# Performance work log

Hardware: AMD Instinct MI355X
Metric: run time of the kernel (lower is better)

Reference implementation:

```python
import jax, jax.numpy as jnp
import numpy as np

N = 20000
E = 640000
IN_DIM = 128
HID = 128
OUT = 64


def setup_inputs() -> dict:
    key = jax.random.key(0)
    ks = jax.random.split(key, 16)
    s = 0.05
    inp = {
        'feat': jax.random.normal(ks[0], (N, IN_DIM), jnp.float32),
        'edge_index': jax.random.randint(ks[1], (2, E), 0, N, jnp.int64),
        # GCNConv params
        'W_gcn': jax.random.normal(ks[2], (IN_DIM, HID), jnp.float32) * s,
        'b_gcn': jnp.zeros((HID,), jnp.float32),
        # SAGEConv params (lin_l: aggregated neighbors w/ bias; lin_r: root, no bias)
        'W_sage_l': jax.random.normal(ks[3], (HID, HID), jnp.float32) * s,
        'b_sage_l': jnp.zeros((HID,), jnp.float32),
        'W_sage_r': jax.random.normal(ks[4], (HID, HID), jnp.float32) * s,
        # policy MLP
        'W1': jax.random.normal(ks[5], (HID, HID), jnp.float32) * s,
        'b1': jnp.zeros((HID,), jnp.float32),
        'W2': jax.random.normal(ks[6], (HID, HID), jnp.float32) * s,
        'b2': jnp.zeros((HID,), jnp.float32),
        'W3': jax.random.normal(ks[7], (HID, OUT), jnp.float32) * s,
        'b3': jnp.zeros((OUT,), jnp.float32),
        # value head
        'Wv': jax.random.normal(ks[8], (HID, 1), jnp.float32) * s,
        'bv': jnp.zeros((1,), jnp.float32),
    }
    return inp


def _gcn(feat, src, dst, W, b):
    # PyG GCNConv: add self loops, sym-normalize by deg^-1/2 on both ends
    loop = jnp.arange(N, dtype=src.dtype)
    s = jnp.concatenate([src, loop])
    d = jnp.concatenate([dst, loop])
    deg = jax.ops.segment_sum(jnp.ones_like(d, jnp.float32), d, num_segments=N)
    dinv = jnp.where(deg > 0, jax.lax.rsqrt(deg), 0.0)
    x = feat @ W  # [N, HID]
    msg = x[s] * (dinv[s] * dinv[d])[:, None]  # [E+N, HID]
    return jax.ops.segment_sum(msg, d, num_segments=N) + b


def _sage_mean(h, src, dst, Wl, bl, Wr):
    # PyG SAGEConv(aggr='mean'): lin_l(mean_neigh) + lin_r(root)
    neigh_sum = jax.ops.segment_sum(h[src], dst, num_segments=N)
    cnt = jax.ops.segment_sum(jnp.ones_like(dst, jnp.float32), dst, num_segments=N)
    mean = neigh_sum / jnp.maximum(cnt, 1.0)[:, None]
    return mean @ Wl + bl + h @ Wr


def reference(feat, edge_index, W_gcn, b_gcn, W_sage_l, b_sage_l, W_sage_r,
              W1, b1, W2, b2, W3, b3, Wv, bv):
    src, dst = edge_index[0], edge_index[1]
    h = jax.nn.relu(_gcn(feat, src, dst, W_gcn, b_gcn))
    h = jax.nn.relu(_sage_mean(h, src, dst, W_sage_l, b_sage_l, W_sage_r))
    # policy MLP (GELU exact, matching torch nn.GELU default)
    z = jax.nn.gelu(h @ W1 + b1, approximate=False)
    z = jax.nn.gelu(z @ W2 + b2, approximate=False)
    means = z @ W3 + b3  # [N, OUT]
    values = (h @ Wv + bv)[:, 0]  # [N]
    return (means, values)
```

## Files before the change

kernel.cpp:

```cpp
#include <hip/hip_runtime.h>
#include <math.h>


typedef __attribute__((ext_vector_type(8))) short short8;
typedef __attribute__((ext_vector_type(4))) float floatx4;

__device__ __forceinline__ unsigned short f2b(float f) {
    unsigned u = __float_as_uint(f);
    unsigned r = (u + 0x7fffu + ((u >> 16) & 1u)) >> 16;
    return (unsigned short)r;
}
__device__ __forceinline__ float b2f(unsigned short h) {
    return __uint_as_float(((unsigned)h) << 16);
}
__device__ __forceinline__ float b2f_lo(unsigned v) {
    return __uint_as_float(v << 16);
}
__device__ __forceinline__ float b2f_hi(unsigned v) {
    return __uint_as_float(v & 0xffff0000u);
}
__device__ __forceinline__ floatx4 MFMA(short8 a, short8 b, floatx4 c) {
    return __builtin_amdgcn_mfma_f32_16x16x32_bf16(a, b, c, 0, 0, 0);
}
__device__ __forceinline__ float gelu_exact(float x) {
    return 0.5f * x * (1.0f + erff(x * 0.70710678118654752440f));
}

#define FRAG(P, ct, ks, lane) (*(const short8*)((P) + (((((ct)*4 + (ks))*64) + (lane)) << 3)))


__global__ __launch_bounds__(256) void count_pack_kernel(
    const int* __restrict__ eidx, int E,
    int* __restrict__ cnt, int* __restrict__ rank,
    const float* Wg, const float* Wsl, const float* Wsr,
    const float* W1, const float* W2, const float* W3,
    unsigned short* Pg, unsigned short* Psl, unsigned short* Psr,
    unsigned short* P1, unsigned short* P2, unsigned short* P3,
    int countBlocks)
{
    if ((int)blockIdx.x < countBlocks) {
        int e = blockIdx.x * 256 + threadIdx.x;
        if (e < E) {
            int d = eidx[E + e];
            rank[e] = atomicAdd(&cnt[d], 1);
        }
        return;
    }
    int t = (blockIdx.x - countBlocks) * 256 + threadIdx.x;
    const float* W; unsigned short* P; int NC = 128; int base;
    if (t < 2048)       { W = Wg;  P = Pg;  base = t; }
    else if (t < 4096)  { W = Wsl; P = Psl; base = t - 2048; }
    else if (t < 6144)  { W = Wsr; P = Psr; base = t - 4096; }
    else if (t < 8192)  { W = W1;  P = P1;  base = t - 6144; }
    else if (t < 10240) { W = W2;  P = P2;  base = t - 8192; }
    else if (t < 11264) { W = W3;  P = P3;  base = t - 10240; NC = 64; }
    else return;
    int l  = base & 63;
    int ks = (base >> 6) & 3;
    int ct = base >> 8;
    int n  = ct * 16 + (l & 15);
    int k0 = ks * 32 + ((l >> 4) << 3);
    short8 v;
    #pragma unroll
    for (int j = 0; j < 8; j++) v[j] = (short)f2b(W[(size_t)(k0 + j) * NC + n]);
    *(short8*)(P + ((size_t)base << 3)) = v;
}


__global__ __launch_bounds__(256) void scan_kernel(
    const int* __restrict__ cnt, int N,
    int* __restrict__ row_ptr, int* __restrict__ bsums,
    float* __restrict__ dinv)
{
    __shared__ int sh[256];
    int b = blockIdx.x, tid = threadIdx.x;
    int i0 = b * 1024 + tid * 4;
    int v0 = (i0 + 0 < N) ? cnt[i0 + 0] : 0;
    int v1 = (i0 + 1 < N) ? cnt[i0 + 1] : 0;
    int v2 = (i0 + 2 < N) ? cnt[i0 + 2] : 0;
    int v3 = (i0 + 3 < N) ? cnt[i0 + 3] : 0;
    int tot = v0 + v1 + v2 + v3;
    sh[tid] = tot;
    __syncthreads();
    for (int off = 1; off < 256; off <<= 1) {
        int t = (tid >= off) ? sh[tid - off] : 0;
        __syncthreads();
        sh[tid] += t;
        __syncthreads();
    }
    int excl = sh[tid] - tot;
    if (i0 + 0 < N) { row_ptr[i0 + 0] = excl;                dinv[i0 + 0] = rsqrtf((float)(v0 + 1)); }
    if (i0 + 1 < N) { row_ptr[i0 + 1] = excl + v0;           dinv[i0 + 1] = rsqrtf((float)(v1 + 1)); }
    if (i0 + 2 < N) { row_ptr[i0 + 2] = excl + v0 + v1;      dinv[i0 + 2] = rsqrtf((float)(v2 + 1)); }
    if (i0 + 3 < N) { row_ptr[i0 + 3] = excl + v0 + v1 + v2; dinv[i0 + 3] = rsqrtf((float)(v3 + 1)); }
    if (tid == 255) bsums[b] = sh[255];
}


__global__ __launch_bounds__(256) void fill_gemm_kernel(
    const int* __restrict__ eidx, const int* __restrict__ rank,
    const int* __restrict__ row_ptr, const int* __restrict__ bsums,
    int E, int* __restrict__ col,
    const float* __restrict__ feat, const unsigned short* __restrict__ Pg,
    unsigned short* __restrict__ xs, int M, int fillBlocks)
{
    if ((int)blockIdx.x < fillBlocks) {
        int e = blockIdx.x * 256 + threadIdx.x;
        if (e < E) {
            int d = eidx[E + e];
            int b = d >> 10;
            int off = 0;
            for (int j = 0; j < b; j++) off += bsums[j];
            col[off + row_ptr[d] + rank[e]] = eidx[e];
        }
        return;
    }
    int bid = blockIdx.x - fillBlocks;
    int w = bid * 4 + (threadIdx.x >> 6);
    if (w >= (M / 16) * 2) return;
    int lane = threadIdx.x & 63;
    int m = lane & 15, quad = lane >> 4;
    int rt = w >> 1, ch = w & 1;
    const float* arow = feat + (size_t)(rt * 16 + m) * 128;
    short8 a[4];
    #pragma unroll
    for (int ks = 0; ks < 4; ks++) {
        float4 f0 = *(const float4*)(arow + ks * 32 + quad * 8);
        float4 f1 = *(const float4*)(arow + ks * 32 + quad * 8 + 4);
        short8 s;
        s[0] = (short)f2b(f0.x); s[1] = (short)f2b(f0.y);
        s[2] = (short)f2b(f0.z); s[3] = (short)f2b(f0.w);
        s[4] = (short)f2b(f1.x); s[5] = (short)f2b(f1.y);
        s[6] = (short)f2b(f1.z); s[7] = (short)f2b(f1.w);
        a[ks] = s;
    }
    #pragma unroll
    for (int ct = 0; ct < 4; ct++) {
        floatx4 acc = {0.f, 0.f, 0.f, 0.f};
        #pragma unroll
        for (int ks = 0; ks < 4; ks++)
            acc = MFMA(a[ks], FRAG(Pg, ch * 4 + ct, ks, lane), acc);
        #pragma unroll
        for (int reg = 0; reg < 4; reg++)
            xs[(size_t)(rt * 16 + quad * 4 + reg) * 128 + (ch * 4 + ct) * 16 + m] =
                f2b(acc[reg]);
    }
}


template<bool GCN>
__global__ __launch_bounds__(256) void agg_kernel(
    const unsigned short* __restrict__ X, const int* __restrict__ row_ptr,
    const int* __restrict__ bsums, const int* __restrict__ col,
    const float* __restrict__ dinv, const float* __restrict__ bias,
    unsigned short* __restrict__ Y, int N, int E)
{
    int w = (int)((blockIdx.x * 256 + threadIdx.x) >> 6);
    if (w >= N) return;
    int lane = threadIdx.x & 63;
    int g = lane >> 4, t = lane & 15;
    const uint4* Xq = (const uint4*)X;

    int b = w >> 10;
    int off = 0;
    for (int j = 0; j < b; j++) off += bsums[j];
    int beg = off + row_ptr[w];
    int end;
    if (w + 1 < N) {
        int off2 = (((w + 1) >> 10) != b) ? off + bsums[b] : off;
        end = off2 + row_ptr[w + 1];
    } else end = E;
    int deg = end - beg;

    float acc[8] = {0.f, 0.f, 0.f, 0.f, 0.f, 0.f, 0.f, 0.f};

    for (int base = beg; base < end; base += 64) {
        int rem = end - base;
        int n = rem < 64 ? rem : 64;
        int idx = (lane < n) ? col[base + lane] : 0;
        for (int j0 = 0; j0 < n; j0 += 16) {
            #pragma unroll
            for (int u = 0; u < 4; u++) {
                int j = j0 + u * 4 + g;
                int s = __shfl(idx, j & 63);
                if (j < n) {
                    uint4 q = Xq[(size_t)s * 16 + t];
                    float sc = GCN ? dinv[s] : 1.0f;
                    acc[0] = fmaf(b2f_lo(q.x), sc, acc[0]);
                    acc[1] = fmaf(b2f_hi(q.x), sc, acc[1]);
                    acc[2] = fmaf(b2f_lo(q.y), sc, acc[2]);
                    acc[3] = fmaf(b2f_hi(q.y), sc, acc[3]);
                    acc[4] = fmaf(b2f_lo(q.z), sc, acc[4]);
                    acc[5] = fmaf(b2f_hi(q.z), sc, acc[5]);
                    acc[6] = fmaf(b2f_lo(q.w), sc, acc[6]);
                    acc[7] = fmaf(b2f_hi(q.w), sc, acc[7]);
                }
            }
        }
    }
    #pragma unroll
    for (int i = 0; i < 8; i++) {
        acc[i] += __shfl_xor(acc[i], 16);
        acc[i] += __shfl_xor(acc[i], 32);
    }
    if (g == 0) {
        float out[8];
        if (GCN) {
            float dw = dinv[w];
            uint4 q = Xq[(size_t)w * 16 + t];
            acc[0] = fmaf(b2f_lo(q.x), dw, acc[0]);
            acc[1] = fmaf(b2f_hi(q.x), dw, acc[1]);
            acc[2] = fmaf(b2f_lo(q.y), dw, acc[2]);
            acc[3] = fmaf(b2f_hi(q.y), dw, acc[3]);
            acc[4] = fmaf(b2f_lo(q.z), dw, acc[4]);
            acc[5] = fmaf(b2f_hi(q.z), dw, acc[5]);
            acc[6] = fmaf(b2f_lo(q.w), dw, acc[6]);
            acc[7] = fmaf(b2f_hi(q.w), dw, acc[7]);
            float4 b0 = *(const float4*)(bias + t * 8);
            float4 b1 = *(const float4*)(bias + t * 8 + 4);
            out[0] = fmaxf(fmaf(acc[0], dw, b0.x), 0.f);
            out[1] = fmaxf(fmaf(acc[1], dw, b0.y), 0.f);
            out[2] = fmaxf(fmaf(acc[2], dw, b0.z), 0.f);
            out[3] = fmaxf(fmaf(acc[3], dw, b0.w), 0.f);
            out[4] = fmaxf(fmaf(acc[4], dw, b1.x), 0.f);
            out[5] = fmaxf(fmaf(acc[5], dw, b1.y), 0.f);
            out[6] = fmaxf(fmaf(acc[6], dw, b1.z), 0.f);
            out[7] = fmaxf(fmaf(acc[7], dw, b1.w), 0.f);
        } else {
            float rc = 1.0f / (float)(deg > 0 ? deg : 1);
            #pragma unroll
            for (int i = 0; i < 8; i++) out[i] = acc[i] * rc;
        }
        uint4 r;
        r.x = (unsigned)f2b(out[0]) | ((unsigned)f2b(out[1]) << 16);
        r.y = (unsigned)f2b(out[2]) | ((unsigned)f2b(out[3]) << 16);
        r.z = (unsigned)f2b(out[4]) | ((unsigned)f2b(out[5]) << 16);
        r.w = (unsigned)f2b(out[6]) | ((unsigned)f2b(out[7]) << 16);
        ((uint4*)Y)[(size_t)w * 16 + t] = r;
    }
}


__global__ __launch_bounds__(256) void sage_mlp_kernel(
    const unsigned short* __restrict__ mean, const unsigned short* __restrict__ h1,
    const unsigned short* __restrict__ Psl, const unsigned short* __restrict__ Psr,
    const float* __restrict__ bsl,
    const unsigned short* __restrict__ P1, const float* __restrict__ b1,
    const unsigned short* __restrict__ P2, const float* __restrict__ b2,
    const unsigned short* __restrict__ P3, const float* __restrict__ b3,
    const float* __restrict__ Wv, const float* __restrict__ bv,
    float* __restrict__ means, float* __restrict__ values, int M)
{
    __shared__ unsigned short z[4][16 * 136];
    int widx = threadIdx.x >> 6, lane = threadIdx.x & 63;
    int w = blockIdx.x * 4 + widx;
    if (w >= M / 16) return;
    int m = lane & 15, quad = lane >> 4;
    unsigned short* zt = &z[widx][0];
    int r0 = w * 16;

    short8 am[4], ar[4];
    #pragma unroll
    for (int ks = 0; ks < 4; ks++) {
        am[ks] = *(const short8*)(mean + (size_t)(r0 + m) * 128 + ks * 32 + quad * 8);
        ar[ks] = *(const short8*)(h1   + (size_t)(r0 + m) * 128 + ks * 32 + quad * 8);
    }

    float vpart[4] = {0.f, 0.f, 0.f, 0.f};
    #pragma unroll
    for (int ct = 0; ct < 8; ct++) {
        floatx4 acc = {0.f, 0.f, 0.f, 0.f};
        #pragma unroll
        for (int ks = 0; ks < 4; ks++) acc = MFMA(am[ks], FRAG(Psl, ct, ks, lane), acc);
        #pragma unroll
        for (int ks = 0; ks < 4; ks++) acc = MFMA(ar[ks], FRAG(Psr, ct, ks, lane), acc);
        float bb = bsl[ct * 16 + m];
        float wv = Wv[ct * 16 + m];
        #pragma unroll
        for (int reg = 0; reg < 4; reg++) {
            float o = fmaxf(acc[reg] + bb, 0.f);
            vpart[reg] = fmaf(o, wv, vpart[reg]);
            zt[(quad * 4 + reg) * 136 + ct * 16 + m] = f2b(o);
        }
    }
    #pragma unroll
    for (int off = 1; off <= 8; off <<= 1) {
        #pragma unroll
        for (int reg = 0; reg < 4; reg++)
            vpart[reg] += __shfl_xor(vpart[reg], off);
    }
    if (m == 0) {
        float bvv = bv[0];
        #pragma unroll
        for (int reg = 0; reg < 4; reg++)
            values[r0 + quad * 4 + reg] = vpart[reg] + bvv;
    }

    short8 a1[4];
    #pragma unroll
    for (int ks = 0; ks < 4; ks++)
        a1[ks] = *(const short8*)(zt + m * 136 + ks * 32 + quad * 8);

    #pragma unroll
    for (int ct = 0; ct < 8; ct++) {
        floatx4 acc = {0.f, 0.f, 0.f, 0.f};
        #pragma unroll
        for (int ks = 0; ks < 4; ks++) acc = MFMA(a1[ks], FRAG(P1, ct, ks, lane), acc);
        float bb = b1[ct * 16 + m];
        #pragma unroll
        for (int reg = 0; reg < 4; reg++)
            zt[(quad * 4 + reg) * 136 + ct * 16 + m] = f2b(gelu_exact(acc[reg] + bb));
    }
    short8 a2[4];
    #pragma unroll
    for (int ks = 0; ks < 4; ks++)
        a2[ks] = *(const short8*)(zt + m * 136 + ks * 32 + quad * 8);

    #pragma unroll
    for (int ct = 0; ct < 8; ct++) {
        floatx4 acc = {0.f, 0.f, 0.f, 0.f};
        #pragma unroll
        for (int ks = 0; ks < 4; ks++) acc = MFMA(a2[ks], FRAG(P2, ct, ks, lane), acc);
        float bb = b2[ct * 16 + m];
        #pragma unroll
        for (int reg = 0; reg < 4; reg++)
            zt[(quad * 4 + reg) * 136 + ct * 16 + m] = f2b(gelu_exact(acc[reg] + bb));
    }
    short8 a3[4];
    #pragma unroll
    for (int ks = 0; ks < 4; ks++)
        a3[ks] = *(const short8*)(zt + m * 136 + ks * 32 + quad * 8);

    #pragma unroll
    for (int ct = 0; ct < 4; ct++) {
        floatx4 acc = {0.f, 0.f, 0.f, 0.f};
        #pragma unroll
        for (int ks = 0; ks < 4; ks++) acc = MFMA(a3[ks], FRAG(P3, ct, ks, lane), acc);
        float bb = b3[ct * 16 + m];
        #pragma unroll
        for (int reg = 0; reg < 4; reg++)
            means[(size_t)(r0 + quad * 4 + reg) * 64 + ct * 16 + m] = acc[reg] + bb;
    }
}


extern "C" void kernel_launch(void* const* d_in, const int* in_sizes, int n_in,
                              void* d_out, int out_size, void* d_ws, size_t ws_size,
                              hipStream_t stream) {
    const float* feat  = (const float*)d_in[0];
    const int*   eidx  = (const int*)d_in[1];
    const float* W_gcn = (const float*)d_in[2];
    const float* b_gcn = (const float*)d_in[3];
    const float* W_sl  = (const float*)d_in[4];
    const float* b_sl  = (const float*)d_in[5];
    const float* W_sr  = (const float*)d_in[6];
    const float* W1    = (const float*)d_in[7];
    const float* b1    = (const float*)d_in[8];
    const float* W2    = (const float*)d_in[9];
    const float* b2    = (const float*)d_in[10];
    const float* W3    = (const float*)d_in[11];
    const float* b3    = (const float*)d_in[12];
    const float* Wv    = (const float*)d_in[13];
    const float* bv    = (const float*)d_in[14];

    const int N = in_sizes[0] / 128;
    const int E = in_sizes[1] / 2;

    char* ws = (char*)d_ws;
    size_t off = 0;
    auto alloc = [&](size_t bytes) -> void* {
        void* p = ws + off;
        off += (bytes + 255) & ~(size_t)255;
        return p;
    };
    int*   cnt     = (int*)alloc((size_t)N * 4);
    int*   rank    = (int*)alloc((size_t)E * 4);
    int*   row_ptr = (int*)alloc((size_t)N * 4);
    int*   bsums   = (int*)alloc(32 * 4);
    float* dinv    = (float*)alloc((size_t)N * 4);
    int*   col     = (int*)alloc((size_t)E * 4);
    unsigned short* xs   = (unsigned short*)alloc((size_t)N * 128 * 2);
    unsigned short* h1   = (unsigned short*)alloc((size_t)N * 128 * 2);
    unsigned short* mean = (unsigned short*)alloc((size_t)N * 128 * 2);
    unsigned short* Pg   = (unsigned short*)alloc(2048 * 8 * 2);
    unsigned short* Psl  = (unsigned short*)alloc(2048 * 8 * 2);
    unsigned short* Psr  = (unsigned short*)alloc(2048 * 8 * 2);
    unsigned short* P1   = (unsigned short*)alloc(2048 * 8 * 2);
    unsigned short* P2   = (unsigned short*)alloc(2048 * 8 * 2);
    unsigned short* P3   = (unsigned short*)alloc(1024 * 8 * 2);

    hipMemsetAsync(cnt, 0, (size_t)N * 4, stream);

    const int countBlocks = (E + 255) / 256;
    const int packBlocks  = (11264 + 255) / 256;
    count_pack_kernel<<<countBlocks + packBlocks, 256, 0, stream>>>(
        eidx, E, cnt, rank, W_gcn, W_sl, W_sr, W1, W2, W3,
        Pg, Psl, Psr, P1, P2, P3, countBlocks);

    const int NB = (N + 1023) / 1024;
    scan_kernel<<<NB, 256, 0, stream>>>(cnt, N, row_ptr, bsums, dinv);

    const int fillBlocks = (E + 255) / 256;
    const int gemmBlocks = ((N / 16) * 2 + 3) / 4;
    fill_gemm_kernel<<<fillBlocks + gemmBlocks, 256, 0, stream>>>(
        eidx, rank, row_ptr, bsums, E, col, feat, Pg, xs, N, fillBlocks);

    const int agrid = (N + 3) / 4;
    agg_kernel<true><<<agrid, 256, 0, stream>>>(xs, row_ptr, bsums, col, dinv, b_gcn, h1, N, E);
    agg_kernel<false><<<agrid, 256, 0, stream>>>(h1, row_ptr, bsums, col, dinv, nullptr, mean, N, E);

    sage_mlp_kernel<<<(N / 16 + 3) / 4, 256, 0, stream>>>(
        mean, h1, Psl, Psr, b_sl, P1, b1, P2, b2, P3, b3, Wv, bv,
        (float*)d_out, (float*)d_out + (size_t)N * 64, N);
}
```

Before: 201.6 us.

## Fuse scan into count kernel, prescale GCN source features, simplify aggregation loop

Merges the degree scan into the count/pack kernel using a last-block-done atomic, and builds the CSR with atomic cursors instead of per-edge ranks plus block offsets. The source-side dinv scaling is folded into the feature GEMM output, so the aggregation loop becomes plain adds with no per-edge dinv gather. The aggregation loop is also rewritten to issue two independent row loads per iteration without shuffles, and row_ptr gets an N+1 sentinel so the per-row offset summation goes away. The costs are a single-block serial scan at the tail of the first kernel, non-deterministic column order within each row, and bf16 rounding applied after the dinv scaling.

Result: slower. 415.9 us (+106.3%).

```diff
diff --git a/kernel.cpp b/kernel.cpp
--- a/kernel.cpp
+++ b/kernel.cpp
@@ -29,89 +29,96 @@
 #define FRAG(P, ct, ks, lane) (*(const short8*)((P) + (((((ct)*4 + (ks))*64) + (lane)) << 3)))
 
 
-__global__ __launch_bounds__(256) void count_pack_kernel(
-    const int* __restrict__ eidx, int E,
-    int* __restrict__ cnt, int* __restrict__ rank,
+__global__ __launch_bounds__(256) void count_pack_scan_kernel(
+    const int* __restrict__ eidx, int E, int N,
+    int* __restrict__ cnt, int* __restrict__ done,
+    int* __restrict__ row_ptr, int* __restrict__ cursor, float* __restrict__ dinv,
     const float* Wg, const float* Wsl, const float* Wsr,
     const float* W1, const float* W2, const float* W3,
     unsigned short* Pg, unsigned short* Psl, unsigned short* Psr,
     unsigned short* P1, unsigned short* P2, unsigned short* P3,
-    int countBlocks)
+    int countBlocks, int totalBlocks)
 {
+    __shared__ int sh[256];
+    __shared__ int isLast;
+
     if ((int)blockIdx.x < countBlocks) {
         int e = blockIdx.x * 256 + threadIdx.x;
-        if (e < E) {
-            int d = eidx[E + e];
-            rank[e] = atomicAdd(&cnt[d], 1);
+        if (e < E) atomicAdd(&cnt[eidx[E + e]], 1);
+    } else {
+        int t = (blockIdx.x - countBlocks) * 256 + threadIdx.x;
+        if (t < 11264) {
+            const float* W; unsigned short* P; int NC = 128; int base;
+            if (t < 2048)       { W = Wg;  P = Pg;  base = t; }
+            else if (t < 4096)  { W = Wsl; P = Psl; base = t - 2048; }
+            else if (t < 6144)  { W = Wsr; P = Psr; base = t - 4096; }
+            else if (t < 8192)  { W = W1;  P = P1;  base = t - 6144; }
+            else if (t < 10240) { W = W2;  P = P2;  base = t - 8192; }
+            else                { W = W3;  P = P3;  base = t - 10240; NC = 64; }
+            int l  = base & 63;
+            int ks = (base >> 6) & 3;
+            int ct = base >> 8;
+            int n  = ct * 16 + (l & 15);
+            int k0 = ks * 32 + ((l >> 4) << 3);
+            short8 v;
+            #pragma unroll
+            for (int j = 0; j < 8; j++) v[j] = (short)f2b(W[(size_t)(k0 + j) * NC + n]);
+            *(short8*)(P + ((size_t)base << 3)) = v;
         }
-        return;
-    }
-    int t = (blockIdx.x - countBlocks) * 256 + threadIdx.x;
-    const float* W; unsigned short* P; int NC = 128; int base;
-    if (t < 2048)       { W = Wg;  P = Pg;  base = t; }
-    else if (t < 4096)  { W = Wsl; P = Psl; base = t - 2048; }
-    else if (t < 6144)  { W = Wsr; P = Psr; base = t - 4096; }
-    else if (t < 8192)  { W = W1;  P = P1;  base = t - 6144; }
-    else if (t < 10240) { W = W2;  P = P2;  base = t - 8192; }
-    else if (t < 11264) { W = W3;  P = P3;  base = t - 10240; NC = 64; }
-    else return;
-    int l  = base & 63;
-    int ks = (base >> 6) & 3;
-    int ct = base >> 8;
-    int n  = ct * 16 + (l & 15);
-    int k0 = ks * 32 + ((l >> 4) << 3);
-    short8 v;
-    #pragma unroll
-    for (int j = 0; j < 8; j++) v[j] = (short)f2b(W[(size_t)(k0 + j) * NC + n]);
-    *(short8*)(P + ((size_t)base << 3)) = v;
-}
-
-
-__global__ __launch_bounds__(256) void scan_kernel(
-    const int* __restrict__ cnt, int N,
-    int* __restrict__ row_ptr, int* __restrict__ bsums,
-    float* __restrict__ dinv)
-{
-    __shared__ int sh[256];
-    int b = blockIdx.x, tid = threadIdx.x;
-    int i0 = b * 1024 + tid * 4;
-    int v0 = (i0 + 0 < N) ? cnt[i0 + 0] : 0;
-    int v1 = (i0 + 1 < N) ? cnt[i0 + 1] : 0;
-    int v2 = (i0 + 2 < N) ? cnt[i0 + 2] : 0;
-    int v3 = (i0 + 3 < N) ? cnt[i0 + 3] : 0;
-    int tot = v0 + v1 + v2 + v3;
-    sh[tid] = tot;
+    }
+
+    __threadfence();
+    __syncthreads();
+    if (threadIdx.x == 0)
+        isLast = (atomicAdd(done, 1) == totalBlocks - 1) ? 1 : 0;
+    __syncthreads();
+    if (!isLast) return;
+    __threadfence();
+
+    int tid = threadIdx.x;
+    int CH = (N + 255) >> 8;
+    int t0 = tid * CH;
+    int sum = 0;
+    for (int i = 0; i < CH; i++) {
+        int idx = t0 + i;
+        if (idx < N) sum += cnt[idx];
+    }
+    sh[tid] = sum;
     __syncthreads();
     for (int off = 1; off < 256; off <<= 1) {
-        int t = (tid >= off) ? sh[tid - off] : 0;
+        int v = (tid >= off) ? sh[tid - off] : 0;
         __syncthreads();
-        sh[tid] += t;
+        sh[tid] += v;
         __syncthreads();
     }
-    int excl = sh[tid] - tot;
-    if (i0 + 0 < N) { row_ptr[i0 + 0] = excl;                dinv[i0 + 0] = rsqrtf((float)(v0 + 1)); }
-    if (i0 + 1 < N) { row_ptr[i0 + 1] = excl + v0;           dinv[i0 + 1] = rsqrtf((float)(v1 + 1)); }
-    if (i0 + 2 < N) { row_ptr[i0 + 2] = excl + v0 + v1;      dinv[i0 + 2] = rsqrtf((float)(v2 + 1)); }
-    if (i0 + 3 < N) { row_ptr[i0 + 3] = excl + v0 + v1 + v2; dinv[i0 + 3] = rsqrtf((float)(v3 + 1)); }
-    if (tid == 255) bsums[b] = sh[255];
+    int run = sh[tid] - sum;
+    for (int i = 0; i < CH; i++) {
+        int idx = t0 + i;
+        if (idx < N) {
+            int c = cnt[idx];
+            row_ptr[idx] = run;
+            cursor[idx]  = run;
+            dinv[idx] = rsqrtf((float)(c + 1));
+            run += c;
+        }
+    }
+    if (tid == 0) row_ptr[N] = E;
 }
 
 
 __global__ __launch_bounds__(256) void fill_gemm_kernel(
-    const int* __restrict__ eidx, const int* __restrict__ rank,
-    const int* __restrict__ row_ptr, const int* __restrict__ bsums,
-    int E, int* __restrict__ col,
-    const float* __restrict__ feat, const unsigned short* __restrict__ Pg,
+    const int* __restrict__ eidx, int E,
+    int* __restrict__ cursor, int* __restrict__ col,
+    const float* __restrict__ feat, const float* __restrict__ dinv,
+    const unsigned short* __restrict__ Pg,
     unsigned short* __restrict__ xs, int M, int fillBlocks)
 {
     if ((int)blockIdx.x < fillBlocks) {
         int e = blockIdx.x * 256 + threadIdx.x;
         if (e < E) {
             int d = eidx[E + e];
-            int b = d >> 10;
-            int off = 0;
-            for (int j = 0; j < b; j++) off += bsums[j];
-            col[off + row_ptr[d] + rank[e]] = eidx[e];
+            int pos = atomicAdd(&cursor[d], 1);
+            col[pos] = eidx[e];
         }
         return;
     }
@@ -134,6 +141,8 @@
         s[6] = (short)f2b(f1.z); s[7] = (short)f2b(f1.w);
         a[ks] = s;
     }
+    float4 dvv = *(const float4*)(dinv + rt * 16 + quad * 4);
+    float dv[4] = {dvv.x, dvv.y, dvv.z, dvv.w};
     #pragma unroll
     for (int ct = 0; ct < 4; ct++) {
         floatx4 acc = {0.f, 0.f, 0.f, 0.f};
@@ -143,7 +152,7 @@
         #pragma unroll
         for (int reg = 0; reg < 4; reg++)
             xs[(size_t)(rt * 16 + quad * 4 + reg) * 128 + (ch * 4 + ct) * 16 + m] =
-                f2b(acc[reg]);
+                f2b(acc[reg] * dv[reg]);
     }
 }
 
@@ -151,9 +160,9 @@
 template<bool GCN>
 __global__ __launch_bounds__(256) void agg_kernel(
     const unsigned short* __restrict__ X, const int* __restrict__ row_ptr,
-    const int* __restrict__ bsums, const int* __restrict__ col,
-    const float* __restrict__ dinv, const float* __restrict__ bias,
-    unsigned short* __restrict__ Y, int N, int E)
+    const int* __restrict__ col, const float* __restrict__ dinv,
+    const float* __restrict__ bias,
+    unsigned short* __restrict__ Y, int N)
 {
     int w = (int)((blockIdx.x * 256 + threadIdx.x) >> 6);
     if (w >= N) return;
@@ -161,43 +170,35 @@
     int g = lane >> 4, t = lane & 15;
     const uint4* Xq = (const uint4*)X;
 
-    int b = w >> 10;
-    int off = 0;
-    for (int j = 0; j < b; j++) off += bsums[j];
-    int beg = off + row_ptr[w];
-    int end;
-    if (w + 1 < N) {
-        int off2 = (((w + 1) >> 10) != b) ? off + bsums[b] : off;
-        end = off2 + row_ptr[w + 1];
-    } else end = E;
+    int beg = row_ptr[w], end = row_ptr[w + 1];
     int deg = end - beg;
 
     float acc[8] = {0.f, 0.f, 0.f, 0.f, 0.f, 0.f, 0.f, 0.f};
 
-    for (int base = beg; base < end; base += 64) {
-        int rem = end - base;
-        int n = rem < 64 ? rem : 64;
-        int idx = (lane < n) ? col[base + lane] : 0;
-        for (int j0 = 0; j0 < n; j0 += 16) {
-            #pragma unroll
-            for (int u = 0; u < 4; u++) {
-                int j = j0 + u * 4 + g;
-                int s = __shfl(idx, j & 63);
-                if (j < n) {
-                    uint4 q = Xq[(size_t)s * 16 + t];
-                    float sc = GCN ? dinv[s] : 1.0f;
-                    acc[0] = fmaf(b2f_lo(q.x), sc, acc[0]);
-                    acc[1] = fmaf(b2f_hi(q.x), sc, acc[1]);
-                    acc[2] = fmaf(b2f_lo(q.y), sc, acc[2]);
-                    acc[3] = fmaf(b2f_hi(q.y), sc, acc[3]);
-                    acc[4] = fmaf(b2f_lo(q.z), sc, acc[4]);
-                    acc[5] = fmaf(b2f_hi(q.z), sc, acc[5]);
-                    acc[6] = fmaf(b2f_lo(q.w), sc, acc[6]);
-                    acc[7] = fmaf(b2f_hi(q.w), sc, acc[7]);
-                }
-            }
-        }
-    }
+    int e = beg + g;
+    for (; e + 4 < end; e += 8) {
+        int s0 = col[e];
+        int s1 = col[e + 4];
+        uint4 q0 = Xq[(size_t)s0 * 16 + t];
+        uint4 q1 = Xq[(size_t)s1 * 16 + t];
+        acc[0] += b2f_lo(q0.x); acc[1] += b2f_hi(q0.x);
+        acc[2] += b2f_lo(q0.y); acc[3] += b2f_hi(q0.y);
+        acc[4] += b2f_lo(q0.z); acc[5] += b2f_hi(q0.z);
+        acc[6] += b2f_lo(q0.w); acc[7] += b2f_hi(q0.w);
+        acc[0] += b2f_lo(q1.x); acc[1] += b2f_hi(q1.x);
+        acc[2] += b2f_lo(q1.y); acc[3] += b2f_hi(q1.y);
+        acc[4] += b2f_lo(q1.z); acc[5] += b2f_hi(q1.z);
+        acc[6] += b2f_lo(q1.w); acc[7] += b2f_hi(q1.w);
+    }
+    if (e < end) {
+        int s0 = col[e];
+        uint4 q0 = Xq[(size_t)s0 * 16 + t];
+        acc[0] += b2f_lo(q0.x); acc[1] += b2f_hi(q0.x);
+        acc[2] += b2f_lo(q0.y); acc[3] += b2f_hi(q0.y);
+        acc[4] += b2f_lo(q0.z); acc[5] += b2f_hi(q0.z);
+        acc[6] += b2f_lo(q0.w); acc[7] += b2f_hi(q0.w);
+    }
+
     #pragma unroll
     for (int i = 0; i < 8; i++) {
         acc[i] += __shfl_xor(acc[i], 16);
@@ -208,14 +209,10 @@
         if (GCN) {
             float dw = dinv[w];
             uint4 q = Xq[(size_t)w * 16 + t];
-            acc[0] = fmaf(b2f_lo(q.x), dw, acc[0]);
-            acc[1] = fmaf(b2f_hi(q.x), dw, acc[1]);
-            acc[2] = fmaf(b2f_lo(q.y), dw, acc[2]);
-            acc[3] = fmaf(b2f_hi(q.y), dw, acc[3]);
-            acc[4] = fmaf(b2f_lo(q.z), dw, acc[4]);
-            acc[5] = fmaf(b2f_hi(q.z), dw, acc[5]);
-            acc[6] = fmaf(b2f_lo(q.w), dw, acc[6]);
-            acc[7] = fmaf(b2f_hi(q.w), dw, acc[7]);
+            acc[0] += b2f_lo(q.x); acc[1] += b2f_hi(q.x);
+            acc[2] += b2f_lo(q.y); acc[3] += b2f_hi(q.y);
+            acc[4] += b2f_lo(q.z); acc[5] += b2f_hi(q.z);
+            acc[6] += b2f_lo(q.w); acc[7] += b2f_hi(q.w);
             float4 b0 = *(const float4*)(bias + t * 8);
             float4 b1 = *(const float4*)(bias + t * 8 + 4);
             out[0] = fmaxf(fmaf(acc[0], dw, b0.x), 0.f);
@@ -373,10 +370,10 @@
         off += (bytes + 255) & ~(size_t)255;
         return p;
     };
-    int*   cnt     = (int*)alloc((size_t)N * 4);
-    int*   rank    = (int*)alloc((size_t)E * 4);
-    int*   row_ptr = (int*)alloc((size_t)N * 4);
-    int*   bsums   = (int*)alloc(32 * 4);
+    int*   cnt     = (int*)alloc((size_t)(N + 64) * 4);
+    int*   done    = cnt + N;
+    int*   row_ptr = (int*)alloc((size_t)(N + 1) * 4);
+    int*   cursor  = (int*)alloc((size_t)N * 4);
     float* dinv    = (float*)alloc((size_t)N * 4);
     int*   col     = (int*)alloc((size_t)E * 4);
     unsigned short* xs   = (unsigned short*)alloc((size_t)N * 128 * 2);
@@ -389,25 +386,24 @@
     unsigned short* P2   = (unsigned short*)alloc(2048 * 8 * 2);
     unsigned short* P3   = (unsigned short*)alloc(1024 * 8 * 2);
 
-    hipMemsetAsync(cnt, 0, (size_t)N * 4, stream);
+    hipMemsetAsync(cnt, 0, (size_t)(N + 64) * 4, stream);
 
     const int countBlocks = (E + 255) / 256;
     const int packBlocks  = (11264 + 255) / 256;
-    count_pack_kernel<<<countBlocks + packBlocks, 256, 0, stream>>>(
-        eidx, E, cnt, rank, W_gcn, W_sl, W_sr, W1, W2, W3,
-        Pg, Psl, Psr, P1, P2, P3, countBlocks);
-
-    const int NB = (N + 1023) / 1024;
-    scan_kernel<<<NB, 256, 0, stream>>>(cnt, N, row_ptr, bsums, dinv);
+    const int totalBlocks = countBlocks + packBlocks;
+    count_pack_scan_kernel<<<totalBlocks, 256, 0, stream>>>(
+        eidx, E, N, cnt, done, row_ptr, cursor, dinv,
+        W_gcn, W_sl, W_sr, W1, W2, W3,
+        Pg, Psl, Psr, P1, P2, P3, countBlocks, totalBlocks);
 
     const int fillBlocks = (E + 255) / 256;
     const int gemmBlocks = ((N / 16) * 2 + 3) / 4;
     fill_gemm_kernel<<<fillBlocks + gemmBlocks, 256, 0, stream>>>(
-        eidx, rank, row_ptr, bsums, E, col, feat, Pg, xs, N, fillBlocks);
+        eidx, E, cursor, col, feat, dinv, Pg, xs, N, fillBlocks);
 
     const int agrid = (N + 3) / 4;
-    agg_kernel<true><<<agrid, 256, 0, stream>>>(xs, row_ptr, bsums, col, dinv, b_gcn, h1, N, E);
-    agg_kernel<false><<<agrid, 256, 0, stream>>>(h1, row_ptr, bsums, col, dinv, nullptr, mean, N, E);
+    agg_kernel<true><<<agrid, 256, 0, stream>>>(xs, row_ptr, col, dinv, b_gcn, h1, N);
+    agg_kernel<false><<<agrid, 256, 0, stream>>>(h1, row_ptr, col, dinv, nullptr, mean, N);
 
     sage_mlp_kernel<<<(N / 16 + 3) / 4, 256, 0, stream>>>(
         mean, h1, Psl, Psr, b_sl, P1, b1, P2, b2, P3, b3, Wv, bv,
```
